# Kernel tuning notes

Hardware: AMD Instinct MI355X
Metric: run time of the kernel (lower is better)

The kernel has to match this reference:

```python
import jax, jax.numpy as jnp
import numpy as np

EPS = 1.0 / 137.0
NUM_HEADS = 16


def yat_dense(x, kernel, bias, alpha):
    y = jnp.einsum('btc,cf->btf', x, kernel)
    x2 = jnp.sum(x * x, axis=-1, keepdims=True)          # [B,T,1]
    k2 = jnp.sum(kernel * kernel, axis=0)                 # [F]
    y = (y * y) / (x2 + k2 - 2.0 * y + EPS)
    out_f = kernel.shape[1]
    scale = (jnp.sqrt(jnp.float32(out_f)) / jnp.log1p(jnp.float32(out_f))) ** alpha
    return y * scale + bias


def setup_inputs() -> dict:
    key = jax.random.key(0)
    ks = jax.random.split(key, 6)
    B, T, C = 2, 1024, 1024
    x = jax.random.normal(ks[0], (B, T, C), dtype=jnp.float32)
    mask = jnp.tril(jnp.ones((T, T), dtype=bool))[None, None, :, :]  # causal [1,1,T,T]
    w_qkv = jax.random.normal(ks[1], (C, 3 * C), dtype=jnp.float32) * 0.02
    b_qkv = jnp.zeros((3 * C,), dtype=jnp.float32)
    alpha_qkv = jnp.ones((1,), dtype=jnp.float32)
    w_proj = jax.random.normal(ks[2], (C, C), dtype=jnp.float32) * 0.02
    b_proj = jnp.zeros((C,), dtype=jnp.float32)
    alpha_proj = jnp.ones((1,), dtype=jnp.float32)
    alpha_attn = jnp.ones((1,), dtype=jnp.float32)
    return {"x": x, "mask": mask, "w_qkv": w_qkv, "b_qkv": b_qkv,
            "alpha_qkv": alpha_qkv, "w_proj": w_proj, "b_proj": b_proj,
            "alpha_proj": alpha_proj, "alpha_attn": alpha_attn}


def reference(x, mask, w_qkv, b_qkv, alpha_qkv, w_proj, b_proj, alpha_proj, alpha_attn):
    B, T, C = x.shape
    head_dim = C // NUM_HEADS
    scale = jnp.log1p(jnp.float32(head_dim))
    inv_scale = (head_dim / scale) ** alpha_attn  # [1]

    qkv = yat_dense(x, w_qkv, b_qkv, alpha_qkv)               # [B,T,3C]
    qkv = qkv.reshape(B, T, 3, NUM_HEADS, head_dim)
    q, k, v = jnp.moveaxis(qkv, 2, 0)                         # each [B,T,H,hd]
    # NOTE: source transposes with (0,3,1,2) -> [B, head_dim, T, H]; reproduced faithfully.
    q = jnp.transpose(q, (0, 3, 1, 2))
    k = jnp.transpose(k, (0, 3, 1, 2))
    v = jnp.transpose(v, (0, 3, 1, 2))

    dot = jnp.einsum('bhid,bhjd->bhij', q, k)                 # [B,hd,T,T]
    sq_dot = dot * dot
    q2 = jnp.sum(q * q, axis=-1, keepdims=True)               # [B,hd,T,1]
    k2 = jnp.sum(k * k, axis=-1, keepdims=True).transpose(0, 1, 3, 2)  # [B,hd,1,T]
    sq_dist = q2 + k2 - 2.0 * dot
    attn = sq_dot / (sq_dist + EPS)
    attn = attn * inv_scale
    attn = jnp.where(mask, attn, jnp.finfo(jnp.float32).min)
    attn = jax.nn.softmax(attn, axis=-1)

    out = jnp.einsum('bhij,bhjd->bhid', attn, v)              # [B,hd,T,H]
    out = out.transpose(0, 2, 1, 3).reshape(B, T, C)
    out = yat_dense(out, w_proj, b_proj, alpha_proj)
    return out
```

## Files before the change

### kernel.cpp

```cpp
#include <hip/hip_runtime.h>
#include <math.h>

#define YAT_EPS (1.0f / 137.0f)


typedef __bf16 bf16x8 __attribute__((ext_vector_type(8)));
typedef float floatx4 __attribute__((ext_vector_type(4)));
typedef unsigned int uintx4 __attribute__((ext_vector_type(4)));

__device__ __forceinline__ float fast_rcp(float x) {
#if __has_builtin(__builtin_amdgcn_rcpf)
    return __builtin_amdgcn_rcpf(x);
#else
    return 1.0f / x;
#endif
}
__device__ __forceinline__ float fast_exp2(float x) {
#if __has_builtin(__builtin_amdgcn_exp2f)
    return __builtin_amdgcn_exp2f(x);
#else
    return exp2f(x);
#endif
}

__device__ __forceinline__ unsigned short f32_bf16(float f) {
    unsigned u = __builtin_bit_cast(unsigned, f);
    u += 0x7fffu + ((u >> 16) & 1u);
    return (unsigned short)(u >> 16);
}
__device__ __forceinline__ float bf16_f32(unsigned short h) {
    unsigned u = ((unsigned)h) << 16;
    return __builtin_bit_cast(float, u);
}

__global__ __launch_bounds__(256) void prep_kernel(
    const float* __restrict__ x,
    const float* __restrict__ w_qkv, const float* __restrict__ w_proj,
    unsigned short* __restrict__ xh, unsigned short* __restrict__ xl,
    float* __restrict__ x2x,
    unsigned short* __restrict__ WtQh, unsigned short* __restrict__ WtQl,
    float* __restrict__ k2q,
    unsigned short* __restrict__ WtPh, unsigned short* __restrict__ WtPl,
    float* __restrict__ k2p,
    float* __restrict__ x2a)
{
    __shared__ float t[32][33];
    const int bid = blockIdx.x;
    const int tid = threadIdx.x;

    if (bid < 4096) {
        const bool isQ = bid < 3072;
        const float* W = isQ ? w_qkv : w_proj;
        unsigned short* th = isQ ? WtQh : WtPh;
        unsigned short* tl = isQ ? WtQl : WtPl;
        float* k2 = isQ ? k2q : k2p;
        const int N = isQ ? 3072 : 1024;
        const int id2 = isQ ? bid : bid - 3072;
        const int nx = isQ ? (id2 % 96) : (id2 & 31);
        const int ky = isQ ? (id2 / 96) : (id2 >> 5);
        const int tx = tid & 31, ty = tid >> 5;
        const int n0 = nx * 32, k0 = ky * 32;
        #pragma unroll
        for (int r = 0; r < 4; ++r)
            t[ty + r * 8][tx] = W[(size_t)(k0 + ty + r * 8) * N + n0 + tx];
        __syncthreads();
        const int tx2 = tid & 15, ty2 = tid >> 4;
        #pragma unroll
        for (int r = 0; r < 2; ++r) {
            const int nl = ty2 + r * 16;
            const int nn = n0 + nl;
            int nw = nn;
            if (isQ) {
                nw = (nn & ~1023) | (((nn & 63) >> 3) << 7)
                   | (((nn >> 6) & 15) << 3) | (nn & 7);
            }
            const float v0 = t[2 * tx2][nl];
            const float v1 = t[2 * tx2 + 1][nl];
            const unsigned short h0 = f32_bf16(v0);
            const unsigned short h1 = f32_bf16(v1);
            *(ushort2*)(th + (size_t)nw * 1024 + k0 + 2 * tx2) =
                make_ushort2(h0, h1);
            *(ushort2*)(tl + (size_t)nw * 1024 + k0 + 2 * tx2) =
                make_ushort2(f32_bf16(v0 - bf16_f32(h0)),
                             f32_bf16(v1 - bf16_f32(h1)));
            float s = fmaf(v0, v0, v1 * v1);
            #pragma unroll
            for (int m = 8; m > 0; m >>= 1) s += __shfl_xor(s, m, 16);
            if (tx2 == 0) atomicAdd(&k2[nn], s);
        }
    } else {
        const int row = bid - 4096;
        float* red = &t[0][0];
        float4 v = *(const float4*)(x + (size_t)row * 1024 + tid * 4);
        float vv[4] = {v.x, v.y, v.z, v.w};
        unsigned short hh[4], ll[4];
        float s = 0.0f;
        #pragma unroll
        for (int e = 0; e < 4; ++e) {
            hh[e] = f32_bf16(vv[e]);
            ll[e] = f32_bf16(vv[e] - bf16_f32(hh[e]));
            s = fmaf(vv[e], vv[e], s);
        }
        *(ushort4*)(xh + (size_t)row * 1024 + tid * 4) =
            make_ushort4(hh[0], hh[1], hh[2], hh[3]);
        *(ushort4*)(xl + (size_t)row * 1024 + tid * 4) =
            make_ushort4(ll[0], ll[1], ll[2], ll[3]);
        #pragma unroll
        for (int off = 32; off > 0; off >>= 1) s += __shfl_down(s, off, 64);
        if ((tid & 63) == 0) red[tid >> 6] = s;
        __syncthreads();
        if (tid == 0) {
            x2x[row] = red[0] + red[1] + red[2] + red[3];
            x2a[row] = 0.0f;
        }
    }
}

template <int BM, int BN, int BK, int MODE, int MINW>
__global__ __launch_bounds__(256, MINW) void gemm_yat_mfma_kernel(
    const unsigned short* __restrict__ Ah, const unsigned short* __restrict__ Al,
    const unsigned short* __restrict__ Bh, const unsigned short* __restrict__ Bl,
    const float* __restrict__ bias, const float* __restrict__ x2,
    const float* __restrict__ k2, const float* __restrict__ alphap,
    float* __restrict__ out, int N, int K, float scale_base,
    unsigned short* __restrict__ kvu, float* __restrict__ q2k,
    float* __restrict__ k2k)
{
    constexpr int TM = (BM / 2) / 16;
    constexpr int TN = (BN / 2) / 16;
    constexpr int ASZ = BM * BK;
    constexpr int BSZ = BN * BK;
    constexpr int AB  = ASZ * 2;
    constexpr int BB  = BSZ * 2;
    constexpr int NI  = (BM + BN) * BK / 1024;
    constexpr int LPR = BK / 8;
    __shared__ __align__(16) unsigned short sbuf[2 * (ASZ + BSZ)];

    const int tid = threadIdx.x;
    const int w = tid >> 6, l = tid & 63;
    const int lane16 = l & 15, quad = l >> 4;
    const int wm = w & 1, wn = w >> 1;
    const int m0 = blockIdx.y * BM, n0 = blockIdx.x * BN;

    floatx4 acc[TM][TN];
    #pragma unroll
    for (int tm = 0; tm < TM; ++tm)
        #pragma unroll
        for (int tn = 0; tn < TN; ++tn)
            acc[tm][tn] = (floatx4){0.f, 0.f, 0.f, 0.f};

    for (int k0 = 0; k0 < K; k0 += BK) {
        __syncthreads();
        #pragma unroll
        for (int i = 0; i < NI; ++i) {
            const int o = (i * 4 + w) * 1024;
            const unsigned short* gp;
            if (o < 2 * AB) {
                const unsigned short* g = (o < AB) ? Ah : Al;
                const int oo = o & (AB - 1);
                gp = g + (size_t)(m0 + oo / (BK * 2) + l / LPR) * K
                       + k0 + (l % LPR) * 8;
            } else {
                const int ob = o - 2 * AB;
                const unsigned short* g = (ob < BB) ? Bh : Bl;
                const int oo = ob & (BB - 1);
                gp = g + (size_t)(n0 + oo / (BK * 2) + l / LPR) * K
                       + k0 + (l % LPR) * 8;
            }
            __builtin_amdgcn_global_load_lds(
                (const __attribute__((address_space(1))) unsigned int*)gp,
                (__attribute__((address_space(3))) unsigned int*)((char*)sbuf + o),
                16, 0, 0);
        }
        __syncthreads();

        #pragma unroll
        for (int kk = 0; kk < BK / 32; ++kk) {
            bf16x8 afh[TM], afl[TM], bfh[TN], bfl[TN];
            #pragma unroll
            for (int tm = 0; tm < TM; ++tm) {
                const int base = (wm * (BM / 2) + tm * 16 + lane16) * BK
                               + kk * 32 + quad * 8;
                afh[tm] = *(const bf16x8*)(sbuf + base);
                afl[tm] = *(const bf16x8*)(sbuf + ASZ + base);
            }
            #pragma unroll
            for (int tn = 0; tn < TN; ++tn) {
                const int nb = (wn * (BN / 2) + tn * 16 + lane16) * BK
                             + kk * 32 + quad * 8;
                bfh[tn] = *(const bf16x8*)(sbuf + 2 * ASZ + nb);
                bfl[tn] = *(const bf16x8*)(sbuf + 2 * ASZ + BSZ + nb);
            }
            #pragma unroll
            for (int tm = 0; tm < TM; ++tm)
                #pragma unroll
                for (int tn = 0; tn < TN; ++tn) {
                    acc[tm][tn] = __builtin_amdgcn_mfma_f32_16x16x32_bf16(
                        afh[tm], bfh[tn], acc[tm][tn], 0, 0, 0);
                    acc[tm][tn] = __builtin_amdgcn_mfma_f32_16x16x32_bf16(
                        afh[tm], bfl[tn], acc[tm][tn], 0, 0, 0);
                    acc[tm][tn] = __builtin_amdgcn_mfma_f32_16x16x32_bf16(
                        afl[tm], bfh[tn], acc[tm][tn], 0, 0, 0);
                }
        }
    }

    const float scale = powf(scale_base, alphap[0]);

    if (MODE == 0) {
        #pragma unroll
        for (int tm = 0; tm < TM; ++tm) {
            #pragma unroll
            for (int tn = 0; tn < TN; ++tn) {
                const int n = n0 + wn * (BN / 2) + tn * 16 + lane16;
                const float kk = k2[n];
                const float bb = bias[n];
                const int mrow = m0 + wm * (BM / 2) + tm * 16 + quad * 4;
                #pragma unroll
                for (int r = 0; r < 4; ++r) {
                    const float y = acc[tm][tn][r];
                    const float den = x2[mrow + r] + kk - 2.0f * y + YAT_EPS;
                    out[(size_t)(mrow + r) * N + n] =
                        y * y / den * scale + bb;
                }
            }
        }
    } else {
        constexpr int G = BM / 32;
        float* lds = (float*)sbuf;
        const int s_ = n0 >> 10;
        const int dblk = (n0 >> 7) & 7;
        const int b_ = m0 >> 10;
        const int tl = tid >> 3;
        const int ddr = tid & 7;
        const int d_glob = dblk * 8 + ddr;

        #pragma unroll
        for (int g = 0; g < G; ++g) {
            __syncthreads();
            if constexpr (G == 1) {
                #pragma unroll
                for (int tn = 0; tn < TN; ++tn) {
                    const int n = n0 + wn * (BN / 2) + tn * 16 + lane16;
                    const int hcol = (n >> 3) & 15;
                    const int norig = (n & ~1023) | (hcol << 6)
                                    | (dblk << 3) | (n & 7);
                    const float kk = k2[norig];
                    const float bb = bias[norig];
                    const int mrow = m0 + wm * 16 + quad * 4;
                    const int tbase = wm * 16 + quad * 4;
                    const int col = wn * (BN / 2) + tn * 16 + lane16;
                    #pragma unroll
                    for (int r = 0; r < 4; ++r) {
                        const float y = acc[0][tn][r];
                        const float den =
                            x2[mrow + r] + kk - 2.0f * y + YAT_EPS;
                        lds[(tbase + r) * 132 + col] =
                            y * y / den * scale + bb;
                    }
                }
            } else {
                constexpr int GH = (G > 1) ? (G / 2) : 1;
                if (wm == g / GH) {
                    const int gl = g % GH;
                    #pragma unroll
                    for (int tm2 = 0; tm2 < 2; ++tm2) {
                        const int tm = gl * 2 + tm2;
                        #pragma unroll
                        for (int tn = 0; tn < TN; ++tn) {
                            const int n = n0 + wn * (BN / 2) + tn * 16 + lane16;
                            const int hcol = (n >> 3) & 15;
                            const int norig = (n & ~1023) | (hcol << 6)
                                            | (dblk << 3) | (n & 7);
                            const float kk = k2[norig];
                            const float bb = bias[norig];
                            const int mrow =
                                m0 + wm * (BM / 2) + tm * 16 + quad * 4;
                            const int tbase = tm2 * 16 + quad * 4;
                            const int col = wn * (BN / 2) + tn * 16 + lane16;
                            #pragma unroll
                            for (int r = 0; r < 4; ++r) {
                                const float y = acc[tm][tn][r];
                                const float den =
                                    x2[mrow + r] + kk - 2.0f * y + YAT_EPS;
                                lds[(tbase + r) * 132 + col] =
                                    y * y / den * scale + bb;
                            }
                        }
                    }
                }
            }
            __syncthreads();

            float y[16];
            #pragma unroll
            for (int h = 0; h < 16; ++h)
                y[h] = lds[tl * 132 + h * 8 + ddr];
            const int t_glob = (m0 & 1023) + g * 32 + tl;

            if (s_ < 2) {
                unsigned short hb[16], lb[16];
                float s2 = 0.f;
                #pragma unroll
                for (int h = 0; h < 16; ++h) {
                    hb[h] = f32_bf16(y[h]);
                    lb[h] = f32_bf16(y[h] - bf16_f32(hb[h]));
                    s2 = fmaf(y[h], y[h], s2);
                }
                unsigned short* dst = kvu + (size_t)b_ * 6291456
                    + (s_ == 0 ? 4194304u : 0u)
                    + ((size_t)(d_glob * 1024 + t_glob)) * 32;
                #pragma unroll
                for (int h4 = 0; h4 < 4; ++h4) {
                    *(ushort4*)(dst + h4 * 4) = make_ushort4(
                        hb[h4*4], hb[h4*4+1], hb[h4*4+2], hb[h4*4+3]);
                    *(ushort4*)(dst + 16 + h4 * 4) = make_ushort4(
                        lb[h4*4], lb[h4*4+1], lb[h4*4+2], lb[h4*4+3]);
                }
                float* sq = (s_ == 0) ? q2k : k2k;
                sq[b_ * 65536 + d_glob * 1024 + t_glob] = s2;
            } else {
                const int j = t_glob;
                const int jt2 = j >> 5;
                const int e = ((j >> 4) & 1) * 4 + (j & 3);
                const int qd = (j >> 2) & 3;
                unsigned short* dst = kvu + (size_t)b_ * 6291456 + 2097152
                    + d_glob * 32768 + jt2 * 1024 + qd * 128 + e;
                #pragma unroll
                for (int h = 0; h < 16; ++h) {
                    const unsigned short vh = f32_bf16(y[h]);
                    dst[h * 8] = vh;
                    dst[512 + h * 8] = f32_bf16(y[h] - bf16_f32(vh));
                }
            }
        }
    }
}

__global__ __launch_bounds__(256, 4) void yat_attn_mfma2_kernel(
    const unsigned short* __restrict__ KVU,
    const float* __restrict__ k2k, const float* __restrict__ q2k,
    const float* __restrict__ alphap,
    unsigned short* __restrict__ attn_h, unsigned short* __restrict__ attn_l,
    float* __restrict__ x2a)
{
    const int tid = threadIdx.x;
    const int lane = tid & 63, w = tid >> 6;
    const int lane16 = lane & 15, quad = lane >> 4;
    const int d = blockIdx.x, c = blockIdx.y, b = blockIdx.z;

    const float isc =
        powf(64.0f / log1pf(64.0f), alphap[0]) * 1.44269504f;

    const unsigned short* kp = KVU + (size_t)b * 6291456 + d * 32768;
    const unsigned short* vp = KVU + (size_t)b * 6291456 + 2097152 + d * 32768;
    const unsigned short* qp = KVU + (size_t)b * 6291456 + 4194304 + d * 32768;
    const float* k2bd = k2k + b * 65536 + d * 1024;
    const float* q2bd = q2k + b * 65536 + d * 1024;

    const int ti0 = c * 4 + w;
    const int tiA = ti0, tiB = 63 - ti0;

    const bf16x8 qA = *(const bf16x8*)(qp + (tiA * 16 + lane16) * 32 + quad * 8);
    const bf16x8 qB = *(const bf16x8*)(qp + (tiB * 16 + lane16) * 32 + quad * 8);
    const float q2A = q2bd[tiA * 16 + lane16] + YAT_EPS;
    const float q2B = q2bd[tiB * 16 + lane16] + YAT_EPS;
    const int iA = tiA * 16 + lane16;
    const int iB = tiB * 16 + lane16;

    floatx4 OA = (floatx4){0.f, 0.f, 0.f, 0.f};
    floatx4 OB = (floatx4){0.f, 0.f, 0.f, 0.f};
    float lsA = 0.f, lsB = 0.f;

    const int lastA = tiA >> 1, lastB = tiB >> 1;

    for (int jt2 = 0; jt2 <= lastB; ++jt2) {
        const int j0 = jt2 * 32;
        const unsigned short* kp0 = kp + (j0 + lane16) * 32;
        const unsigned short* kp1 = kp + (j0 + 16 + lane16) * 32;
        const bf16x8 k0a = *(const bf16x8*)(kp0 + quad * 8);
        const bf16x8 k0b = *(const bf16x8*)(kp0 + ((quad ^ 2) * 8));
        const bf16x8 k1a = *(const bf16x8*)(kp1 + quad * 8);
        const bf16x8 k1b = *(const bf16x8*)(kp1 + ((quad ^ 2) * 8));
        const unsigned short* vpj = vp + jt2 * 1024 + quad * 128 + lane16 * 8;
        const bf16x8 vh = *(const bf16x8*)(vpj);
        const bf16x8 vl = *(const bf16x8*)(vpj + 512);
        const float4 k20 = *(const float4*)(k2bd + j0 + quad * 4);
        const float4 k21 = *(const float4*)(k2bd + j0 + 16 + quad * 4);
        const float k2r[8] = {k20.x, k20.y, k20.z, k20.w,
                              k21.x, k21.y, k21.z, k21.w};
        const int jbase0 = j0 + quad * 4;

        #pragma unroll
        for (int half = 0; half < 2; ++half) {
            if (half == 0 && jt2 > lastA) continue;
            const bf16x8 qf = half ? qB : qA;
            const float q2e = half ? q2B : q2A;
            const int iM = half ? iB : iA;
            const int tiH = half ? tiB : tiA;

            __builtin_amdgcn_s_setprio(1);
            floatx4 S0 = __builtin_amdgcn_mfma_f32_16x16x32_bf16(
                k0a, qf, (floatx4){0.f, 0.f, 0.f, 0.f}, 0, 0, 0);
            S0 = __builtin_amdgcn_mfma_f32_16x16x32_bf16(k0b, qf, S0, 0, 0, 0);
            floatx4 S1 = __builtin_amdgcn_mfma_f32_16x16x32_bf16(
                k1a, qf, (floatx4){0.f, 0.f, 0.f, 0.f}, 0, 0, 0);
            S1 = __builtin_amdgcn_mfma_f32_16x16x32_bf16(k1b, qf, S1, 0, 0, 0);
            __builtin_amdgcn_s_setprio(0);

            float p[8], lsum = 0.f;
            if (j0 + 31 <= tiH * 16) {
                #pragma unroll
                for (int e = 0; e < 8; ++e) {
                    const float s = (e < 4) ? S0[e & 3] : S1[e & 3];
                    const float den = fmaf(-2.f, s, q2e + k2r[e]);
                    const float pe = fast_exp2(s * s * fast_rcp(den) * isc);
                    lsum += pe;
                    p[e] = pe;
                }
            } else {
                #pragma unroll
                for (int e = 0; e < 8; ++e) {
                    const float s = (e < 4) ? S0[e & 3] : S1[e & 3];
                    const int j = jbase0 + (e >> 2) * 16 + (e & 3);
                    const float den = fmaf(-2.f, s, q2e + k2r[e]);
                    float pe = fast_exp2(s * s * fast_rcp(den) * isc);
                    pe = (j <= iM) ? pe : 0.f;
                    lsum += pe;
                    p[e] = pe;
                }
            }
            if (half) lsB += lsum; else lsA += lsum;

            unsigned ph32[4], pl32[4];
            #pragma unroll
            for (int e2 = 0; e2 < 4; ++e2) {
                const unsigned b0 = __builtin_bit_cast(unsigned, p[e2 * 2]);
                const unsigned b1 = __builtin_bit_cast(unsigned, p[e2 * 2 + 1]);
                ph32[e2] = __builtin_amdgcn_perm(b1, b0, 0x07060302u);
                const float f0 = p[e2 * 2] -
                    __builtin_bit_cast(float, b0 & 0xFFFF0000u);
                const float f1 = p[e2 * 2 + 1] -
                    __builtin_bit_cast(float, b1 & 0xFFFF0000u);
                pl32[e2] = __builtin_amdgcn_perm(
                    __builtin_bit_cast(unsigned, f1),
                    __builtin_bit_cast(unsigned, f0), 0x07060302u);
            }
            const bf16x8 Ph = __builtin_bit_cast(bf16x8,
                (uintx4){ph32[0], ph32[1], ph32[2], ph32[3]});
            const bf16x8 Pl = __builtin_bit_cast(bf16x8,
                (uintx4){pl32[0], pl32[1], pl32[2], pl32[3]});

            floatx4 O = half ? OB : OA;
            __builtin_amdgcn_s_setprio(1);
            O = __builtin_amdgcn_mfma_f32_16x16x32_bf16(Ph, vh, O, 0, 0, 0);
            O = __builtin_amdgcn_mfma_f32_16x16x32_bf16(Pl, vh, O, 0, 0, 0);
            O = __builtin_amdgcn_mfma_f32_16x16x32_bf16(Ph, vl, O, 0, 0, 0);
            __builtin_amdgcn_s_setprio(0);
            if (half) OB = O; else OA = O;
        }
    }

    #pragma unroll
    for (int half = 0; half < 2; ++half) {
        float ls = half ? lsB : lsA;
        const floatx4 O = half ? OB : OA;
        const int ti = half ? tiB : tiA;
        ls += __shfl_xor(ls, 16, 64);
        ls += __shfl_xor(ls, 32, 64);
        const float linv = 1.0f / ls;
        #pragma unroll
        for (int r = 0; r < 4; ++r) {
            const float lr = __shfl(linv, quad * 4 + r, 16);
            const float v = O[r] * lr;
            const int i = ti * 16 + quad * 4 + r;
            const size_t off =
                ((size_t)(b * 1024 + i)) * 1024 + d * 16 + lane16;
            const unsigned short vh16 = f32_bf16(v);
            attn_h[off] = vh16;
            attn_l[off] = f32_bf16(v - bf16_f32(vh16));
            float s2 = v * v;
            s2 += __shfl_xor(s2, 1, 64);
            s2 += __shfl_xor(s2, 2, 64);
            s2 += __shfl_xor(s2, 4, 64);
            s2 += __shfl_xor(s2, 8, 64);
            if (lane16 == 0) atomicAdd(&x2a[b * 1024 + i], s2);
        }
    }
}

extern "C" void kernel_launch(void* const* d_in, const int* in_sizes, int n_in,
                              void* d_out, int out_size, void* d_ws, size_t ws_size,
                              hipStream_t stream)
{
    const float* x          = (const float*)d_in[0];
    const float* w_qkv      = (const float*)d_in[2];
    const float* b_qkv      = (const float*)d_in[3];
    const float* alpha_qkv  = (const float*)d_in[4];
    const float* w_proj     = (const float*)d_in[5];
    const float* b_proj     = (const float*)d_in[6];
    const float* alpha_proj = (const float*)d_in[7];
    const float* alpha_attn = (const float*)d_in[8];
    float* out = (float*)d_out;

    float* ws = (float*)d_ws;
    unsigned short* KVU  = (unsigned short*)ws;
    unsigned short* WtQh = (unsigned short*)(ws + 6291456);
    unsigned short* WtQl = (unsigned short*)(ws + 7864320);
    unsigned short* WtPh = (unsigned short*)(ws + 9437184);
    unsigned short* WtPl = (unsigned short*)(ws + 9961472);
    unsigned short* xh   = (unsigned short*)(ws + 10485760);
    unsigned short* xl   = (unsigned short*)(ws + 11534336);
    float* x2x  = ws + 12582912;
    float* x2a  = ws + 12584960;
    float* k2q  = ws + 12587008;
    float* k2p  = ws + 12590080;
    float* k2k  = ws + 12591104;
    float* q2k  = ws + 12722176;
    unsigned short* attn_h = WtQh;
    unsigned short* attn_l = WtQl;

    hipMemsetAsync(k2q, 0, (3072 + 1024) * sizeof(float), stream);

    prep_kernel<<<6144, 256, 0, stream>>>(
        x, w_qkv, w_proj, xh, xl, x2x, WtQh, WtQl, k2q, WtPh, WtPl, k2p, x2a);

    const float sb_qkv = sqrtf(3072.0f) / log1pf(3072.0f);
    gemm_yat_mfma_kernel<64, 128, 64, 2, 3><<<dim3(24, 32), 256, 0, stream>>>(
        xh, xl, WtQh, WtQl, b_qkv, x2x, k2q, alpha_qkv, nullptr,
        3072, 1024, sb_qkv, KVU, q2k, k2k);

    yat_attn_mfma2_kernel<<<dim3(64, 8, 2), 256, 0, stream>>>(
        KVU, k2k, q2k, alpha_attn, attn_h, attn_l, x2a);

    const float sb_proj = sqrtf(1024.0f) / log1pf(1024.0f);
    gemm_yat_mfma_kernel<64, 64, 64, 0, 2><<<dim3(16, 32), 256, 0, stream>>>(
        attn_h, attn_l, WtPh, WtPl, b_proj, x2a, k2p, alpha_proj, out,
        1024, 1024, sb_proj, nullptr, nullptr, nullptr);
}
```

Before: 219.9 us.

## Split-K the projection GEMM into two partials with a fused yat epilogue fixup

The output projection GEMM now splits its K dimension across two grid z-slices. Each slice writes raw fp32 partial sums into workspace that the attention stage no longer needs. A new fixup kernel adds the two partials and applies the yat-dense epilogue (squared dot over distance, scale, bias). This doubles the block count of a small 512-block GEMM to fill more CUs, at the cost of an extra kernel launch and a round trip of 16 MB of partials through memory.

```diff
diff --git a/kernel.cpp b/kernel.cpp
--- a/kernel.cpp
+++ b/kernel.cpp
@@ -141,6 +141,8 @@
     const int lane16 = l & 15, quad = l >> 4;
     const int wm = w & 1, wn = w >> 1;
     const int m0 = blockIdx.y * BM, n0 = blockIdx.x * BN;
+    const int kspan = K / gridDim.z;
+    const int kbeg = blockIdx.z * kspan;
 
     floatx4 acc[TM][TN];
     #pragma unroll
@@ -149,7 +151,7 @@
         for (int tn = 0; tn < TN; ++tn)
             acc[tm][tn] = (floatx4){0.f, 0.f, 0.f, 0.f};
 
-    for (int k0 = 0; k0 < K; k0 += BK) {
+    for (int k0 = kbeg; k0 < kbeg + kspan; k0 += BK) {
         __syncthreads();
         #pragma unroll
         for (int i = 0; i < NI; ++i) {
@@ -205,9 +207,25 @@
         }
     }
 
+    if constexpr (MODE == 1) {
+        const size_t zoff = (size_t)blockIdx.z * 2048 * N;
+        #pragma unroll
+        for (int tm = 0; tm < TM; ++tm) {
+            #pragma unroll
+            for (int tn = 0; tn < TN; ++tn) {
+                const int n = n0 + wn * (BN / 2) + tn * 16 + lane16;
+                const int mrow = m0 + wm * (BM / 2) + tm * 16 + quad * 4;
+                #pragma unroll
+                for (int r = 0; r < 4; ++r)
+                    out[zoff + (size_t)(mrow + r) * N + n] = acc[tm][tn][r];
+            }
+        }
+        return;
+    }
+
     const float scale = powf(scale_base, alphap[0]);
 
-    if (MODE == 0) {
+    if constexpr (MODE == 0) {
         #pragma unroll
         for (int tm = 0; tm < TM; ++tm) {
             #pragma unroll
@@ -225,7 +243,7 @@
                 }
             }
         }
-    } else {
+    } else if constexpr (MODE == 2) {
         constexpr int G = BM / 32;
         float* lds = (float*)sbuf;
         const int s_ = n0 >> 10;
@@ -337,6 +355,41 @@
     }
 }
 
+__global__ __launch_bounds__(256) void proj_fixup_kernel(
+    const float* __restrict__ part, const float* __restrict__ x2,
+    const float* __restrict__ k2, const float* __restrict__ bias,
+    const float* __restrict__ alphap, float* __restrict__ out,
+    float scale_base)
+{
+    const float scale = powf(scale_base, alphap[0]);
+    const int g = blockIdx.x * 256 + threadIdx.x;
+    const int row = g >> 8;
+    const int c4 = (g & 255) * 4;
+    const float4 a = ((const float4*)part)[g];
+    const float4 b = ((const float4*)part)[g + 524288];
+    const float4 kk = *(const float4*)(k2 + c4);
+    const float4 bb = *(const float4*)(bias + c4);
+    const float xr = x2[row] + YAT_EPS;
+    float4 o;
+    {
+        const float y = a.x + b.x;
+        o.x = y * y / (xr + kk.x - 2.0f * y) * scale + bb.x;
+    }
+    {
+        const float y = a.y + b.y;
+        o.y = y * y / (xr + kk.y - 2.0f * y) * scale + bb.y;
+    }
+    {
+        const float y = a.z + b.z;
+        o.z = y * y / (xr + kk.z - 2.0f * y) * scale + bb.z;
+    }
+    {
+        const float y = a.w + b.w;
+        o.w = y * y / (xr + kk.w - 2.0f * y) * scale + bb.w;
+    }
+    ((float4*)out)[g] = o;
+}
+
 __global__ __launch_bounds__(256, 4) void yat_attn_mfma2_kernel(
     const unsigned short* __restrict__ KVU,
     const float* __restrict__ k2k, const float* __restrict__ q2k,
@@ -519,6 +572,7 @@
     float* q2k  = ws + 12722176;
     unsigned short* attn_h = WtQh;
     unsigned short* attn_l = WtQl;
+    float* projp = ws;
 
     hipMemsetAsync(k2q, 0, (3072 + 1024) * sizeof(float), stream);
 
@@ -534,7 +588,10 @@
         KVU, k2k, q2k, alpha_attn, attn_h, attn_l, x2a);
 
     const float sb_proj = sqrtf(1024.0f) / log1pf(1024.0f);
-    gemm_yat_mfma_kernel<64, 64, 64, 0, 2><<<dim3(16, 32), 256, 0, stream>>>(
-        attn_h, attn_l, WtPh, WtPl, b_proj, x2a, k2p, alpha_proj, out,
+    gemm_yat_mfma_kernel<64, 64, 64, 1, 4><<<dim3(16, 32, 2), 256, 0, stream>>>(
+        attn_h, attn_l, WtPh, WtPl, b_proj, x2a, k2p, alpha_proj, projp,
         1024, 1024, sb_proj, nullptr, nullptr, nullptr);
-}
+
+    proj_fixup_kernel<<<2048, 256, 0, stream>>>(
+        projp, x2a, k2p, b_proj, alpha_proj, out, sb_proj);
+}
```

New measurement: 223.4 us. No clear change (+1.6%).

## Assign one query tile per wave in attention kernel, doubling grid

Applied to the files above, without the earlier changes.

The attention kernel stops pairing tile ti with tile 63-ti inside each wave, which had balanced causal work. Each wave now handles a single 16-row query tile, the grid doubles along y, and launch bounds go from 4 to 8 blocks per CU to raise occupancy and cut registers. The trade is that causal work is now uneven across waves and blocks, and each K/V fragment load is reused by one tile instead of two. A small GEMM epilogue cleanup folds the G==1 branch into the general path.

```diff
diff --git a/kernel.cpp b/kernel.cpp
--- a/kernel.cpp
+++ b/kernel.cpp
@@ -207,7 +207,7 @@
 
     const float scale = powf(scale_base, alphap[0]);
 
-    if (MODE == 0) {
+    if constexpr (MODE == 0) {
         #pragma unroll
         for (int tm = 0; tm < TM; ++tm) {
             #pragma unroll
@@ -238,34 +238,14 @@
         #pragma unroll
         for (int g = 0; g < G; ++g) {
             __syncthreads();
-            if constexpr (G == 1) {
-                #pragma unroll
-                for (int tn = 0; tn < TN; ++tn) {
-                    const int n = n0 + wn * (BN / 2) + tn * 16 + lane16;
-                    const int hcol = (n >> 3) & 15;
-                    const int norig = (n & ~1023) | (hcol << 6)
-                                    | (dblk << 3) | (n & 7);
-                    const float kk = k2[norig];
-                    const float bb = bias[norig];
-                    const int mrow = m0 + wm * 16 + quad * 4;
-                    const int tbase = wm * 16 + quad * 4;
-                    const int col = wn * (BN / 2) + tn * 16 + lane16;
-                    #pragma unroll
-                    for (int r = 0; r < 4; ++r) {
-                        const float y = acc[0][tn][r];
-                        const float den =
-                            x2[mrow + r] + kk - 2.0f * y + YAT_EPS;
-                        lds[(tbase + r) * 132 + col] =
-                            y * y / den * scale + bb;
-                    }
-                }
-            } else {
+            {
                 constexpr int GH = (G > 1) ? (G / 2) : 1;
-                if (wm == g / GH) {
+                if (G == 1 || wm == g / GH) {
                     const int gl = g % GH;
                     #pragma unroll
                     for (int tm2 = 0; tm2 < 2; ++tm2) {
-                        const int tm = gl * 2 + tm2;
+                        const int tm = (G == 1) ? 0 : (gl * 2 + tm2);
+                        if (G == 1 && tm2 == 1) break;
                         #pragma unroll
                         for (int tn = 0; tn < TN; ++tn) {
                             const int n = n0 + wn * (BN / 2) + tn * 16 + lane16;
@@ -274,9 +254,12 @@
                                             | (dblk << 3) | (n & 7);
                             const float kk = k2[norig];
                             const float bb = bias[norig];
-                            const int mrow =
-                                m0 + wm * (BM / 2) + tm * 16 + quad * 4;
-                            const int tbase = tm2 * 16 + quad * 4;
+                            const int mrow = (G == 1)
+                                ? (m0 + wm * 16 + quad * 4)
+                                : (m0 + wm * (BM / 2) + tm * 16 + quad * 4);
+                            const int tbase = (G == 1)
+                                ? (wm * 16 + quad * 4)
+                                : (tm2 * 16 + quad * 4);
                             const int col = wn * (BN / 2) + tn * 16 + lane16;
                             #pragma unroll
                             for (int r = 0; r < 4; ++r) {
@@ -337,7 +320,7 @@
     }
 }
 
-__global__ __launch_bounds__(256, 4) void yat_attn_mfma2_kernel(
+__global__ __launch_bounds__(256, 8) void yat_attn_mfma2_kernel(
     const unsigned short* __restrict__ KVU,
     const float* __restrict__ k2k, const float* __restrict__ q2k,
     const float* __restrict__ alphap,
@@ -358,23 +341,17 @@
     const float* k2bd = k2k + b * 65536 + d * 1024;
     const float* q2bd = q2k + b * 65536 + d * 1024;
 
-    const int ti0 = c * 4 + w;
-    const int tiA = ti0, tiB = 63 - ti0;
-
-    const bf16x8 qA = *(const bf16x8*)(qp + (tiA * 16 + lane16) * 32 + quad * 8);
-    const bf16x8 qB = *(const bf16x8*)(qp + (tiB * 16 + lane16) * 32 + quad * 8);
-    const float q2A = q2bd[tiA * 16 + lane16] + YAT_EPS;
-    const float q2B = q2bd[tiB * 16 + lane16] + YAT_EPS;
-    const int iA = tiA * 16 + lane16;
-    const int iB = tiB * 16 + lane16;
-
-    floatx4 OA = (floatx4){0.f, 0.f, 0.f, 0.f};
-    floatx4 OB = (floatx4){0.f, 0.f, 0.f, 0.f};
-    float lsA = 0.f, lsB = 0.f;
-
-    const int lastA = tiA >> 1, lastB = tiB >> 1;
-
-    for (int jt2 = 0; jt2 <= lastB; ++jt2) {
+    const int ti = c * 4 + w;
+
+    const bf16x8 qf = *(const bf16x8*)(qp + (ti * 16 + lane16) * 32 + quad * 8);
+    const float q2e = q2bd[ti * 16 + lane16] + YAT_EPS;
+    const int iM = ti * 16 + lane16;
+
+    floatx4 O = (floatx4){0.f, 0.f, 0.f, 0.f};
+    float ls = 0.f;
+    const int lastJ = ti >> 1;
+
+    for (int jt2 = 0; jt2 <= lastJ; ++jt2) {
         const int j0 = jt2 * 32;
         const unsigned short* kp0 = kp + (j0 + lane16) * 32;
         const unsigned short* kp1 = kp + (j0 + 16 + lane16) * 32;
@@ -391,101 +368,84 @@
                               k21.x, k21.y, k21.z, k21.w};
         const int jbase0 = j0 + quad * 4;
 
-        #pragma unroll
-        for (int half = 0; half < 2; ++half) {
-            if (half == 0 && jt2 > lastA) continue;
-            const bf16x8 qf = half ? qB : qA;
-            const float q2e = half ? q2B : q2A;
-            const int iM = half ? iB : iA;
-            const int tiH = half ? tiB : tiA;
-
-            __builtin_amdgcn_s_setprio(1);
-            floatx4 S0 = __builtin_amdgcn_mfma_f32_16x16x32_bf16(
-                k0a, qf, (floatx4){0.f, 0.f, 0.f, 0.f}, 0, 0, 0);
-            S0 = __builtin_amdgcn_mfma_f32_16x16x32_bf16(k0b, qf, S0, 0, 0, 0);
-            floatx4 S1 = __builtin_amdgcn_mfma_f32_16x16x32_bf16(
-                k1a, qf, (floatx4){0.f, 0.f, 0.f, 0.f}, 0, 0, 0);
-            S1 = __builtin_amdgcn_mfma_f32_16x16x32_bf16(k1b, qf, S1, 0, 0, 0);
-            __builtin_amdgcn_s_setprio(0);
-
-            float p[8], lsum = 0.f;
-            if (j0 + 31 <= tiH * 16) {
-                #pragma unroll
-                for (int e = 0; e < 8; ++e) {
-                    const float s = (e < 4) ? S0[e & 3] : S1[e & 3];
-                    const float den = fmaf(-2.f, s, q2e + k2r[e]);
-                    const float pe = fast_exp2(s * s * fast_rcp(den) * isc);
-                    lsum += pe;
-                    p[e] = pe;
-                }
-            } else {
-                #pragma unroll
-                for (int e = 0; e < 8; ++e) {
-                    const float s = (e < 4) ? S0[e & 3] : S1[e & 3];
-                    const int j = jbase0 + (e >> 2) * 16 + (e & 3);
-                    const float den = fmaf(-2.f, s, q2e + k2r[e]);
-                    float pe = fast_exp2(s * s * fast_rcp(den) * isc);
-                    pe = (j <= iM) ? pe : 0.f;
-                    lsum += pe;
-                    p[e] = pe;
-                }
-            }
-            if (half) lsB += lsum; else lsA += lsum;
-
-            unsigned ph32[4], pl32[4];
-            #pragma unroll
-            for (int e2 = 0; e2 < 4; ++e2) {
-                const unsigned b0 = __builtin_bit_cast(unsigned, p[e2 * 2]);
-                const unsigned b1 = __builtin_bit_cast(unsigned, p[e2 * 2 + 1]);
-                ph32[e2] = __builtin_amdgcn_perm(b1, b0, 0x07060302u);
-                const float f0 = p[e2 * 2] -
-                    __builtin_bit_cast(float, b0 & 0xFFFF0000u);
-                const float f1 = p[e2 * 2 + 1] -
-                    __builtin_bit_cast(float, b1 & 0xFFFF0000u);
-                pl32[e2] = __builtin_amdgcn_perm(
-                    __builtin_bit_cast(unsigned, f1),
-                    __builtin_bit_cast(unsigned, f0), 0x07060302u);
-            }
-            const bf16x8 Ph = __builtin_bit_cast(bf16x8,
-                (uintx4){ph32[0], ph32[1], ph32[2], ph32[3]});
-            const bf16x8 Pl = __builtin_bit_cast(bf16x8,
-                (uintx4){pl32[0], pl32[1], pl32[2], pl32[3]});
-
-            floatx4 O = half ? OB : OA;
-            __builtin_amdgcn_s_setprio(1);
-            O = __builtin_amdgcn_mfma_f32_16x16x32_bf16(Ph, vh, O, 0, 0, 0);
-            O = __builtin_amdgcn_mfma_f32_16x16x32_bf16(Pl, vh, O, 0, 0, 0);
-            O = __builtin_amdgcn_mfma_f32_16x16x32_bf16(Ph, vl, O, 0, 0, 0);
-            __builtin_amdgcn_s_setprio(0);
-            if (half) OB = O; else OA = O;
-        }
+        __builtin_amdgcn_s_setprio(1);
+        floatx4 S0 = __builtin_amdgcn_mfma_f32_16x16x32_bf16(
+            k0a, qf, (floatx4){0.f, 0.f, 0.f, 0.f}, 0, 0, 0);
+        S0 = __builtin_amdgcn_mfma_f32_16x16x32_bf16(k0b, qf, S0, 0, 0, 0);
+        floatx4 S1 = __builtin_amdgcn_mfma_f32_16x16x32_bf16(
+            k1a, qf, (floatx4){0.f, 0.f, 0.f, 0.f}, 0, 0, 0);
+        S1 = __builtin_amdgcn_mfma_f32_16x16x32_bf16(k1b, qf, S1, 0, 0, 0);
+        __builtin_amdgcn_s_setprio(0);
+
+        float p[8], lsum = 0.f;
+        if (j0 + 31 <= ti * 16) {
+            #pragma unroll
+            for (int e = 0; e < 8; ++e) {
+                const float s = (e < 4) ? S0[e & 3] : S1[e & 3];
+                const float den = fmaf(-2.f, s, q2e + k2r[e]);
+                const float pe = fast_exp2(s * s * fast_rcp(den) * isc);
+                lsum += pe;
+                p[e] = pe;
+            }
+        } else {
+            #pragma unroll
+            for (int e = 0; e < 8; ++e) {
+                const float s = (e < 4) ? S0[e & 3] : S1[e & 3];
+                const int j = jbase0 + (e >> 2) * 16 + (e & 3);
+                const float den = fmaf(-2.f, s, q2e + k2r[e]);
+                float pe = fast_exp2(s * s * fast_rcp(den) * isc);
+                pe = (j <= iM) ? pe : 0.f;
+                lsum += pe;
+                p[e] = pe;
+            }
+        }
+        ls += lsum;
+
+        unsigned ph32[4], pl32[4];
+        #pragma unroll
+        for (int e2 = 0; e2 < 4; ++e2) {
+            const unsigned b0 = __builtin_bit_cast(unsigned, p[e2 * 2]);
+            const unsigned b1 = __builtin_bit_cast(unsigned, p[e2 * 2 + 1]);
+            ph32[e2] = __builtin_amdgcn_perm(b1, b0, 0x07060302u);
+            const float f0 = p[e2 * 2] -
+                __builtin_bit_cast(float, b0 & 0xFFFF0000u);
+            const float f1 = p[e2 * 2 + 1] -
+                __builtin_bit_cast(float, b1 & 0xFFFF0000u);
+            pl32[e2] = __builtin_amdgcn_perm(
+                __builtin_bit_cast(unsigned, f1),
+                __builtin_bit_cast(unsigned, f0), 0x07060302u);
+        }
+        const bf16x8 Ph = __builtin_bit_cast(bf16x8,
+            (uintx4){ph32[0], ph32[1], ph32[2], ph32[3]});
+        const bf16x8 Pl = __builtin_bit_cast(bf16x8,
+            (uintx4){pl32[0], pl32[1], pl32[2], pl32[3]});
+
+        __builtin_amdgcn_s_setprio(1);
+        O = __builtin_amdgcn_mfma_f32_16x16x32_bf16(Ph, vh, O, 0, 0, 0);
+        O = __builtin_amdgcn_mfma_f32_16x16x32_bf16(Pl, vh, O, 0, 0, 0);
+        O = __builtin_amdgcn_mfma_f32_16x16x32_bf16(Ph, vl, O, 0, 0, 0);
+        __builtin_amdgcn_s_setprio(0);
     }
 
+    ls += __shfl_xor(ls, 16, 64);
+    ls += __shfl_xor(ls, 32, 64);
+    const float linv = 1.0f / ls;
     #pragma unroll
-    for (int half = 0; half < 2; ++half) {
-        float ls = half ? lsB : lsA;
-        const floatx4 O = half ? OB : OA;
-        const int ti = half ? tiB : tiA;
-        ls += __shfl_xor(ls, 16, 64);
-        ls += __shfl_xor(ls, 32, 64);
-        const float linv = 1.0f / ls;
-        #pragma unroll
-        for (int r = 0; r < 4; ++r) {
-            const float lr = __shfl(linv, quad * 4 + r, 16);
-            const float v = O[r] * lr;
-            const int i = ti * 16 + quad * 4 + r;
-            const size_t off =
-                ((size_t)(b * 1024 + i)) * 1024 + d * 16 + lane16;
-            const unsigned short vh16 = f32_bf16(v);
-            attn_h[off] = vh16;
-            attn_l[off] = f32_bf16(v - bf16_f32(vh16));
-            float s2 = v * v;
-            s2 += __shfl_xor(s2, 1, 64);
-            s2 += __shfl_xor(s2, 2, 64);
-            s2 += __shfl_xor(s2, 4, 64);
-            s2 += __shfl_xor(s2, 8, 64);
-            if (lane16 == 0) atomicAdd(&x2a[b * 1024 + i], s2);
-        }
+    for (int r = 0; r < 4; ++r) {
+        const float lr = __shfl(linv, quad * 4 + r, 16);
+        const float v = O[r] * lr;
+        const int i = ti * 16 + quad * 4 + r;
+        const size_t off =
+            ((size_t)(b * 1024 + i)) * 1024 + d * 16 + lane16;
+        const unsigned short vh16 = f32_bf16(v);
+        attn_h[off] = vh16;
+        attn_l[off] = f32_bf16(v - bf16_f32(vh16));
+        float s2 = v * v;
+        s2 += __shfl_xor(s2, 1, 64);
+        s2 += __shfl_xor(s2, 2, 64);
+        s2 += __shfl_xor(s2, 4, 64);
+        s2 += __shfl_xor(s2, 8, 64);
+        if (lane16 == 0) atomicAdd(&x2a[b * 1024 + i], s2);
     }
 }
 
@@ -530,7 +490,7 @@
         xh, xl, WtQh, WtQl, b_qkv, x2x, k2q, alpha_qkv, nullptr,
         3072, 1024, sb_qkv, KVU, q2k, k2k);
 
-    yat_attn_mfma2_kernel<<<dim3(64, 8, 2), 256, 0, stream>>>(
+    yat_attn_mfma2_kernel<<<dim3(64, 16, 2), 256, 0, stream>>>(
         KVU, k2k, q2k, alpha_attn, attn_h, attn_l, x2a);
 
     const float sb_proj = sqrtf(1024.0f) / log1pf(1024.0f);
```

Result: slower. 262.3 us (+19.3%).
